# Performance work log

Hardware: AMD Instinct MI355X
Metric: run time of the kernel (lower is better)

Reference implementation:

```python
import jax, jax.numpy as jnp
import numpy as np

B, A, NBH, F, G, H = 8, 512, 64, 128, 50, 8
DH = F // H
CUTOFF = 5.0


def setup_inputs() -> dict:
    key = jax.random.key(0)
    ks = jax.random.split(key, 13)
    x = jax.random.normal(ks[0], (B, A, F), jnp.float32)
    e = jax.random.normal(ks[1], (B, A, F), jnp.float32)
    t = jax.random.normal(ks[2], (B, F), jnp.float32)
    # distances in [0, 1.2*cutoff] so some pairs fall outside the cutoff
    r_ij = jax.random.uniform(ks[3], (B, A, NBH), jnp.float32) * (1.2 * CUTOFF)
    f_ij = jax.random.normal(ks[4], (B, A, NBH, G), jnp.float32)
    neighbors = jax.random.randint(ks[5], (B, A, NBH), 0, A, jnp.int32)
    neighbor_mask = jax.random.randint(ks[6], (B, A, NBH), 0, 2, jnp.int32).astype(bool)
    sF = 1.0 / np.sqrt(F).astype(np.float32)
    W_filt = jax.random.normal(ks[7], (G, F), jnp.float32) * (1.0 / np.sqrt(G).astype(np.float32))
    b_filt = jnp.zeros((F,), jnp.float32)
    Wq = jax.random.normal(ks[8], (F, F), jnp.float32) * sF
    Wk = jax.random.normal(ks[9], (F, F), jnp.float32) * sF
    Wv = jax.random.normal(ks[10], (F, F), jnp.float32) * sF
    Wo = jax.random.normal(ks[11], (F, F), jnp.float32) * sF
    bo = jnp.zeros((F,), jnp.float32)
    return dict(e=e, x=x, t=t, r_ij=r_ij, f_ij=f_ij,
                W_filt=W_filt, b_filt=b_filt, Wq=Wq, Wk=Wk, Wv=Wv, Wo=Wo, bo=bo,
                neighbors=neighbors, neighbor_mask=neighbor_mask)


def reference(e, x, t, r_ij, f_ij, W_filt, b_filt, Wq, Wk, Wv, Wo, bo,
              neighbors, neighbor_mask):
    # ---- filter network + cosine cutoff: W (B, A, NBH, F) ----
    W = f_ij @ W_filt + b_filt
    C = 0.5 * (jnp.cos(jnp.pi * r_ij / CUTOFF) + 1.0)
    C = C * (r_ij < CUTOFF).astype(x.dtype)           # (B, A, NBH)
    W = W * C[..., None]

    # ---- neighbor gather: nbh (B, A, NBH, F) ----
    bidx = jnp.arange(B)[:, None, None]
    nbh = x[bidx, neighbors]                           # irregular gather
    nbh = nbh * W                                      # filter-modulated messages

    # ---- EgoAttention: central atom queries its neighbors ----
    q = (x @ Wq).reshape(B, A, H, DH)                  # bahd
    k = (nbh @ Wk).reshape(B, A, NBH, H, DH)           # banhd
    v = (nbh @ Wv).reshape(B, A, NBH, H, DH)
    scale = np.float32(1.0 / np.sqrt(DH))
    scores = jnp.einsum('bahd,banhd->bahn', q, k) * scale
    scores = jnp.where(neighbor_mask[:, :, None, :], scores, jnp.float32(-1e9))
    attn = jax.nn.softmax(scores, axis=-1)             # over neighbors
    msg = jnp.einsum('bahn,banhd->bahd', attn, v).reshape(B, A, F)
    v_out = msg @ Wo + bo

    # ---- residual (apply_transition_function=False branch) ----
    return x + v_out
```

## Files before the change

### kernel.cpp

```cpp
#include <hip/hip_runtime.h>
#include <math.h>

#define BB 8
#define AA 512
#define NBH 64
#define FF 128
#define GG 50
#define CUTOFF 5.0f

typedef __attribute__((ext_vector_type(8)))  short bf16x8;
typedef __attribute__((ext_vector_type(4)))  float f32x4;
typedef __attribute__((ext_vector_type(16))) float f32x16;

#define MST 136

#define WV_OFF   0
#define WO_OFF   16384
#define WQ_OFF   32768
#define WKT_OFF  49152
#define WF_OFF   65536
#define XB_OFF   73728
#define KQ_OFF   598016
#define PACK_ELEMS 598016
#define PACK_BLOCKS (PACK_ELEMS / 256)
#define QK_BLOCKS  1024

__device__ __forceinline__ short f2bf(float f) {
    union { float f; unsigned u; } v; v.f = f;
    unsigned r = v.u + 0x7fffu + ((v.u >> 16) & 1u);
    return (short)(r >> 16);
}
__device__ __forceinline__ short f2bf_fast(float f) {
    return (short)((__float_as_uint(f) + 0x8000u) >> 16);
}
__device__ __forceinline__ unsigned int pk2bf(float a, float b) {
    unsigned int ua = __float_as_uint(a) + 0x8000u;
    unsigned int ub = __float_as_uint(b) + 0x8000u;
    return __builtin_amdgcn_perm(ub, ua, 0x07060302u);
}
__device__ __forceinline__ bf16x8 ld_f8_bfpk(const float* p) {
    const float2* p2 = (const float2*)p;
    float2 a = p2[0], b = p2[1], c = p2[2], d = p2[3];
    union { unsigned int u[4]; bf16x8 v; } r;
    r.u[0] = pk2bf(a.x, a.y);
    r.u[1] = pk2bf(b.x, b.y);
    r.u[2] = pk2bf(c.x, c.y);
    r.u[3] = pk2bf(d.x, d.y);
    return r.v;
}
__device__ __forceinline__ int swz(int n) { return ((n >> 3) & 3) << 3; }

__global__ void pack_kernel(const float* __restrict__ Wk,
                            const float* __restrict__ Wv,
                            const float* __restrict__ Wq,
                            const float* __restrict__ Wo,
                            const float* __restrict__ Wf,
                            const float* __restrict__ b_filt,
                            const float* __restrict__ x,
                            short* __restrict__ ws)
{
    int gid = blockIdx.x * blockDim.x + threadIdx.x;
    if (gid < 16384) {
        int idx = gid;
        int j = idx & 7, l = (idx >> 3) & 63, rest = idx >> 9;
        int s = rest & 7, w = rest >> 3;
        int k = 16 * s + ((l >> 5) << 3) + j;
        int n = 32 * w + (l & 31);
        ws[WV_OFF + idx] = f2bf(Wv[k * FF + n]);
    } else if (gid < 65536) {
        int which = (gid - 16384) >> 14;
        int idx = (gid - 16384) & 16383;
        int j = idx & 7, l = (idx >> 3) & 63, rest = idx >> 9;
        int s = rest & 3, c = rest >> 2;
        int k = 32 * s + (l >> 4) * 8 + j;
        int n = 16 * c + (l & 15);
        float v;
        if (which == 0)      v = Wo[k * FF + n];
        else if (which == 1) v = Wq[k * FF + n];
        else                 v = Wk[n * FF + k];
        ws[WO_OFF + which * 16384 + idx] = f2bf(v);
    } else if (gid < 73728) {
        int idx = gid - 65536;
        int j = idx & 7, l = (idx >> 3) & 63, rest = idx >> 9;
        int s = rest & 3, w = rest >> 2;
        int k = 16 * s + ((l >> 5) << 3) + j;
        int n = 32 * w + (l & 31);
        float v = (k < GG) ? Wf[k * FF + n] : (k == GG ? b_filt[n] : 0.0f);
        ws[WF_OFF + idx] = f2bf(v);
    } else {
        int idx = gid - XB_OFF;
        ws[XB_OFF + idx] = f2bf(x[idx]);
    }
}

__global__ __launch_bounds__(256)
void qk_kernel(const short* __restrict__ xB,
               const short* __restrict__ WqB,
               const short* __restrict__ WktB,
               short* __restrict__ kqc)
{
    const int tid  = threadIdx.x;
    const int lane = tid & 63;
    const int w    = tid >> 6;
    const int a    = blockIdx.x * 4 + w;
    const int l15  = lane & 15;
    const int quad = lane >> 4;

    __shared__ short qls[4][128];

    {
        const short* xbrow = &xB[(size_t)a * FF];
        bf16x8 xa[4];
#pragma unroll
        for (int s = 0; s < 4; ++s)
            xa[s] = *(const bf16x8*)&xbrow[32 * s + quad * 8];
#pragma unroll
        for (int cg = 0; cg < 8; ++cg) {
            f32x4 z = {0.f, 0.f, 0.f, 0.f};
#pragma unroll
            for (int s = 0; s < 4; ++s) {
                bf16x8 bq = *(const bf16x8*)&WqB[((cg * 4 + s) * 64 + lane) * 8];
                z = __builtin_amdgcn_mfma_f32_16x16x32_bf16(xa[s], bq, z, 0, 0, 0);
            }
            if (quad == 0) qls[w][cg * 16 + l15] = f2bf_fast(z[0] * 0.25f);
        }
    }
    __syncthreads();

    {
        short* kqa = kqc + (size_t)a * 1024;
        bf16x8 zero8;
#pragma unroll
        for (int jj = 0; jj < 8; ++jj) zero8[jj] = 0;
        bf16x8 ap[4];
#pragma unroll
        for (int s = 0; s < 4; ++s) {
            bf16x8 qoct = *(const bf16x8*)&qls[w][32 * s + quad * 8];
            int h8 = 2 * s + (quad >> 1);
            ap[s] = (l15 == h8) ? qoct : zero8;
        }
#pragma unroll
        for (int ct = 0; ct < 8; ++ct) {
            f32x4 z = {0.f, 0.f, 0.f, 0.f};
#pragma unroll
            for (int s = 0; s < 4; ++s) {
                bf16x8 bk = *(const bf16x8*)&WktB[((ct * 4 + s) * 64 + lane) * 8];
                z = __builtin_amdgcn_mfma_f32_16x16x32_bf16(ap[s], bk, z, 0, 0, 0);
            }
            if (quad < 2) {
#pragma unroll
                for (int r = 0; r < 4; ++r) {
                    int h = quad * 4 + r;
                    kqa[h * 128 + ct * 16 + l15] = f2bf_fast(z[r]);
                }
            }
        }
    }
}

__global__ __launch_bounds__(256, 4)
void tdt_main(const float* __restrict__ x,
              const float* __restrict__ r_ij,
              const float* __restrict__ f_ij,
              const float* __restrict__ bo,
              const int*   __restrict__ neighbors,
              const int*   __restrict__ nmask,
              const short* __restrict__ WvB,
              const short* __restrict__ WoB,
              const short* __restrict__ WfB,
              const short* __restrict__ xB,
              const short* __restrict__ kqc,
              float* __restrict__ out)
{
    const int ba   = blockIdx.x;
    const int b    = ba >> 9;
    const int tid  = threadIdx.x;
    const int lane = tid & 63;
    const int w    = tid >> 6;
    const int l15  = lane & 15;
    const int quad = lane >> 4;
    const int l31  = lane & 31;
    const int khalf = (lane >> 5) << 3;
    const int w5_4  = (lane >> 5) * 4;

    __shared__ short M_s[NBH * MST];
    __shared__ short msg_bf[FF];

    const float* xrow = x + (size_t)ba * FF;
    const unsigned short* xbu = (const unsigned short*)xB + (size_t)b * AA * FF;
    const size_t bao = (size_t)ba;

    int   nbr_reg = neighbors[bao * NBH + lane];
    float C_reg;
    {
        float r = r_ij[bao * NBH + lane];
        float c = 0.5f * (__cosf((float)M_PI * r * (1.0f / CUTOFF)) + 1.0f);
        C_reg = (r < CUTOFF) ? c : 0.0f;
    }
    unsigned long long mask64 = __ballot(nmask[bao * NBH + lane] != 0);

    {
        const float* fm0 = f_ij + bao * (size_t)(NBH * GG) + (size_t)l31 * GG;
        int c = 32 * w + l31;
#pragma unroll
        for (int mt = 0; mt < 2; ++mt) {
            f32x16 wacc;
#pragma unroll
            for (int r = 0; r < 16; ++r) wacc[r] = 0.0f;
            const float* fm = fm0 + mt * 32 * GG;
#pragma unroll
            for (int s = 0; s < 4; ++s) {
                bf16x8 bfw = *(const bf16x8*)&WfB[((w * 4 + s) * 64 + lane) * 8];
                bf16x8 fa;
                if (s < 3) {
                    fa = ld_f8_bfpk(fm + 16 * s + khalf);
                } else {
#pragma unroll
                    for (int jj = 0; jj < 8; ++jj) fa[jj] = 0;
                    if (lane < 32) {
                        fa[0] = f2bf_fast(fm[48]);
                        fa[1] = f2bf_fast(fm[49]);
                        fa[2] = (short)0x3F80;
                    }
                }
                wacc = __builtin_amdgcn_mfma_f32_32x32x16_bf16(fa, bfw, wacc, 0, 0, 0);
            }
#pragma unroll
            for (int r = 0; r < 16; ++r) {
                int   n   = 32 * mt + (r & 3) + 8 * (r >> 2) + w5_4;
                int   nbn = __shfl(nbr_reg, n, 64);
                float cn  = __shfl(C_reg, n, 64);
                float xv  = __uint_as_float((unsigned)xbu[(size_t)nbn * FF + c] << 16);
                M_s[n * MST + (c ^ swz(n))] = f2bf_fast(wacc[r] * cn * xv);
            }
        }
    }
    __syncthreads();

    float sum = 0.0f, acc = 0.0f;
    const short* kqa = kqc + (size_t)ba * 1024 + (size_t)(2 * w + ((lane >> 4) & 1)) * 128;
#pragma unroll
    for (int mt = 0; mt < 2; ++mt) {
        int m = 32 * mt + l31;
        f32x16 sacc, vacc;
#pragma unroll
        for (int r = 0; r < 16; ++r) { sacc[r] = 0.0f; vacc[r] = 0.0f; }
#pragma unroll
        for (int s = 0; s < 8; ++s) {
            bf16x8 ma = *(const bf16x8*)&M_s[m * MST + ((16 * s + khalf) ^ swz(m))];
            bf16x8 bq = *(const bf16x8*)&kqa[16 * s + khalf];
            bf16x8 bv = *(const bf16x8*)&WvB[((w * 8 + s) * 64 + lane) * 8];
            sacc = __builtin_amdgcn_mfma_f32_32x32x16_bf16(ma, bq, sacc, 0, 0, 0);
            vacc = __builtin_amdgcn_mfma_f32_32x32x16_bf16(ma, bv, vacc, 0, 0, 0);
        }
#pragma unroll
        for (int r = 0; r < 16; ++r) {
            int   n = 32 * mt + (r & 3) + 8 * (r >> 2) + w5_4;
            float e = ((mask64 >> n) & 1ull) ? __expf(sacc[r]) : 0.0f;
            sum += e;
            acc  = fmaf(e, vacc[r], acc);
        }
    }
    sum += __shfl_xor(sum, 32, 64);
    acc += __shfl_xor(acc, 32, 64);
    if (lane < 32) msg_bf[32 * w + l31] = f2bf_fast(acc / sum);
    __syncthreads();

    {
        bf16x8 mga[4];
#pragma unroll
        for (int s = 0; s < 4; ++s)
            mga[s] = *(const bf16x8*)&msg_bf[s * 32 + quad * 8];
#pragma unroll
        for (int ct = 0; ct < 2; ++ct) {
            int cg = 2 * w + ct;
            f32x4 z = {0.f, 0.f, 0.f, 0.f};
#pragma unroll
            for (int s = 0; s < 4; ++s) {
                bf16x8 bw = *(const bf16x8*)&WoB[((cg * 4 + s) * 64 + lane) * 8];
                z = __builtin_amdgcn_mfma_f32_16x16x32_bf16(mga[s], bw, z, 0, 0, 0);
            }
            if (quad == 0) {
                int col = cg * 16 + l15;
                out[bao * FF + col] = z[0] + xrow[col] + bo[col];
            }
        }
    }
}

extern "C" void kernel_launch(void* const* d_in, const int* in_sizes, int n_in,
                              void* d_out, int out_size, void* d_ws, size_t ws_size,
                              hipStream_t stream) {
    const float* x      = (const float*)d_in[1];
    const float* r_ij   = (const float*)d_in[3];
    const float* f_ij   = (const float*)d_in[4];
    const float* W_filt = (const float*)d_in[5];
    const float* b_filt = (const float*)d_in[6];
    const float* Wq     = (const float*)d_in[7];
    const float* Wk     = (const float*)d_in[8];
    const float* Wv     = (const float*)d_in[9];
    const float* Wo     = (const float*)d_in[10];
    const float* bo     = (const float*)d_in[11];
    const int*   nbr    = (const int*)d_in[12];
    const int*   msk    = (const int*)d_in[13];
    float* out = (float*)d_out;

    short* ws   = (short*)d_ws;
    short* WvB  = ws + WV_OFF;
    short* WoB  = ws + WO_OFF;
    short* WqB  = ws + WQ_OFF;
    short* WktB = ws + WKT_OFF;
    short* WfB  = ws + WF_OFF;
    short* xB   = ws + XB_OFF;
    short* kqc  = ws + KQ_OFF;

    hipLaunchKernelGGL(pack_kernel, dim3(PACK_BLOCKS), dim3(256), 0, stream,
                       Wk, Wv, Wq, Wo, W_filt, b_filt, x, ws);
    hipLaunchKernelGGL(qk_kernel, dim3(QK_BLOCKS), dim3(256), 0, stream,
                       xB, WqB, WktB, kqc);
    hipLaunchKernelGGL(tdt_main, dim3(BB * AA), dim3(256), 0, stream,
                       x, r_ij, f_ij, bo, nbr, msk,
                       WvB, WoB, WfB, xB, kqc, out);
}
```

Before: 170.7 us.

## Merge weight packing and q/k projection into one prep kernel, drop bf16 x copy

```diff
diff --git a/kernel.cpp b/kernel.cpp
--- a/kernel.cpp
+++ b/kernel.cpp
@@ -16,12 +16,9 @@
 
 #define WV_OFF   0
 #define WO_OFF   16384
-#define WQ_OFF   32768
-#define WKT_OFF  49152
-#define WF_OFF   65536
-#define XB_OFF   73728
-#define KQ_OFF   598016
-#define PACK_ELEMS 598016
+#define WF_OFF   32768
+#define KQ_OFF   40960
+#define PACK_ELEMS 40960
 #define PACK_BLOCKS (PACK_ELEMS / 256)
 #define QK_BLOCKS  1024
 
@@ -50,7 +47,7 @@
 }
 __device__ __forceinline__ int swz(int n) { return ((n >> 3) & 3) << 3; }
 
-__global__ void pack_kernel(const float* __restrict__ Wk,
+__global__ void prep_kernel(const float* __restrict__ Wk,
                             const float* __restrict__ Wv,
                             const float* __restrict__ Wq,
                             const float* __restrict__ Wo,
@@ -59,67 +56,59 @@
                             const float* __restrict__ x,
                             short* __restrict__ ws)
 {
-    int gid = blockIdx.x * blockDim.x + threadIdx.x;
-    if (gid < 16384) {
-        int idx = gid;
-        int j = idx & 7, l = (idx >> 3) & 63, rest = idx >> 9;
-        int s = rest & 7, w = rest >> 3;
-        int k = 16 * s + ((l >> 5) << 3) + j;
-        int n = 32 * w + (l & 31);
-        ws[WV_OFF + idx] = f2bf(Wv[k * FF + n]);
-    } else if (gid < 65536) {
-        int which = (gid - 16384) >> 14;
-        int idx = (gid - 16384) & 16383;
-        int j = idx & 7, l = (idx >> 3) & 63, rest = idx >> 9;
-        int s = rest & 3, c = rest >> 2;
-        int k = 32 * s + (l >> 4) * 8 + j;
-        int n = 16 * c + (l & 15);
-        float v;
-        if (which == 0)      v = Wo[k * FF + n];
-        else if (which == 1) v = Wq[k * FF + n];
-        else                 v = Wk[n * FF + k];
-        ws[WO_OFF + which * 16384 + idx] = f2bf(v);
-    } else if (gid < 73728) {
-        int idx = gid - 65536;
-        int j = idx & 7, l = (idx >> 3) & 63, rest = idx >> 9;
-        int s = rest & 3, w = rest >> 2;
-        int k = 16 * s + ((l >> 5) << 3) + j;
-        int n = 32 * w + (l & 31);
-        float v = (k < GG) ? Wf[k * FF + n] : (k == GG ? b_filt[n] : 0.0f);
-        ws[WF_OFF + idx] = f2bf(v);
-    } else {
-        int idx = gid - XB_OFF;
-        ws[XB_OFF + idx] = f2bf(x[idx]);
-    }
-}
-
-__global__ __launch_bounds__(256)
-void qk_kernel(const short* __restrict__ xB,
-               const short* __restrict__ WqB,
-               const short* __restrict__ WktB,
-               short* __restrict__ kqc)
-{
-    const int tid  = threadIdx.x;
+    const int bid = blockIdx.x;
+    const int tid = threadIdx.x;
+
+    __shared__ short qls[4][128];
+
+    if (bid < PACK_BLOCKS) {
+        int gid = bid * 256 + tid;
+        if (gid < 16384) {
+            int idx = gid;
+            int j = idx & 7, l = (idx >> 3) & 63, rest = idx >> 9;
+            int s = rest & 7, w = rest >> 3;
+            int k = 16 * s + ((l >> 5) << 3) + j;
+            int n = 32 * w + (l & 31);
+            ws[WV_OFF + idx] = f2bf(Wv[k * FF + n]);
+        } else if (gid < 32768) {
+            int idx = gid - 16384;
+            int j = idx & 7, l = (idx >> 3) & 63, rest = idx >> 9;
+            int s = rest & 3, c = rest >> 2;
+            int k = 32 * s + (l >> 4) * 8 + j;
+            int n = 16 * c + (l & 15);
+            ws[WO_OFF + idx] = f2bf(Wo[k * FF + n]);
+        } else {
+            int idx = gid - 32768;
+            int j = idx & 7, l = (idx >> 3) & 63, rest = idx >> 9;
+            int s = rest & 3, w = rest >> 2;
+            int k = 16 * s + ((l >> 5) << 3) + j;
+            int n = 32 * w + (l & 31);
+            float v = (k < GG) ? Wf[k * FF + n] : (k == GG ? b_filt[n] : 0.0f);
+            ws[WF_OFF + idx] = f2bf(v);
+        }
+        return;
+    }
+
+    const int w    = tid >> 6;
     const int lane = tid & 63;
-    const int w    = tid >> 6;
-    const int a    = blockIdx.x * 4 + w;
+    const int a    = (bid - PACK_BLOCKS) * 4 + w;
     const int l15  = lane & 15;
     const int quad = lane >> 4;
 
-    __shared__ short qls[4][128];
-
-    {
-        const short* xbrow = &xB[(size_t)a * FF];
+    {
         bf16x8 xa[4];
 #pragma unroll
         for (int s = 0; s < 4; ++s)
-            xa[s] = *(const bf16x8*)&xbrow[32 * s + quad * 8];
+            xa[s] = ld_f8_bfpk(x + (size_t)a * FF + 32 * s + quad * 8);
 #pragma unroll
         for (int cg = 0; cg < 8; ++cg) {
             f32x4 z = {0.f, 0.f, 0.f, 0.f};
 #pragma unroll
             for (int s = 0; s < 4; ++s) {
-                bf16x8 bq = *(const bf16x8*)&WqB[((cg * 4 + s) * 64 + lane) * 8];
+                const float* wq = Wq + (size_t)(32 * s + quad * 8) * FF + 16 * cg + l15;
+                bf16x8 bq;
+#pragma unroll
+                for (int j = 0; j < 8; ++j) bq[j] = f2bf_fast(wq[j * FF]);
                 z = __builtin_amdgcn_mfma_f32_16x16x32_bf16(xa[s], bq, z, 0, 0, 0);
             }
             if (quad == 0) qls[w][cg * 16 + l15] = f2bf_fast(z[0] * 0.25f);
@@ -128,7 +117,7 @@
     __syncthreads();
 
     {
-        short* kqa = kqc + (size_t)a * 1024;
+        short* kqa = ws + KQ_OFF + (size_t)a * 1024;
         bf16x8 zero8;
 #pragma unroll
         for (int jj = 0; jj < 8; ++jj) zero8[jj] = 0;
@@ -144,7 +133,7 @@
             f32x4 z = {0.f, 0.f, 0.f, 0.f};
 #pragma unroll
             for (int s = 0; s < 4; ++s) {
-                bf16x8 bk = *(const bf16x8*)&WktB[((ct * 4 + s) * 64 + lane) * 8];
+                bf16x8 bk = ld_f8_bfpk(Wk + (size_t)(16 * ct + l15) * FF + 32 * s + quad * 8);
                 z = __builtin_amdgcn_mfma_f32_16x16x32_bf16(ap[s], bk, z, 0, 0, 0);
             }
             if (quad < 2) {
@@ -168,7 +157,6 @@
               const short* __restrict__ WvB,
               const short* __restrict__ WoB,
               const short* __restrict__ WfB,
-              const short* __restrict__ xB,
               const short* __restrict__ kqc,
               float* __restrict__ out)
 {
@@ -187,8 +175,8 @@
     __shared__ short msg_bf[FF];
 
     const float* xrow = x + (size_t)ba * FF;
-    const unsigned short* xbu = (const unsigned short*)xB + (size_t)b * AA * FF;
-    const size_t bao = (size_t)ba;
+    const float* xb   = x + (size_t)b * AA * FF;
+    const size_t bao  = (size_t)ba;
 
     int   nbr_reg = neighbors[bao * NBH + lane];
     float C_reg;
@@ -230,7 +218,7 @@
                 int   n   = 32 * mt + (r & 3) + 8 * (r >> 2) + w5_4;
                 int   nbn = __shfl(nbr_reg, n, 64);
                 float cn  = __shfl(C_reg, n, 64);
-                float xv  = __uint_as_float((unsigned)xbu[(size_t)nbn * FF + c] << 16);
+                float xv  = xb[(size_t)nbn * FF + c];
                 M_s[n * MST + (c ^ swz(n))] = f2bf_fast(wacc[r] * cn * xv);
             }
         }
@@ -305,20 +293,15 @@
     const int*   msk    = (const int*)d_in[13];
     float* out = (float*)d_out;
 
-    short* ws   = (short*)d_ws;
-    short* WvB  = ws + WV_OFF;
-    short* WoB  = ws + WO_OFF;
-    short* WqB  = ws + WQ_OFF;
-    short* WktB = ws + WKT_OFF;
-    short* WfB  = ws + WF_OFF;
-    short* xB   = ws + XB_OFF;
-    short* kqc  = ws + KQ_OFF;
-
-    hipLaunchKernelGGL(pack_kernel, dim3(PACK_BLOCKS), dim3(256), 0, stream,
+    short* ws  = (short*)d_ws;
+    short* WvB = ws + WV_OFF;
+    short* WoB = ws + WO_OFF;
+    short* WfB = ws + WF_OFF;
+    short* kqc = ws + KQ_OFF;
+
+    hipLaunchKernelGGL(prep_kernel, dim3(PACK_BLOCKS + QK_BLOCKS), dim3(256), 0, stream,
                        Wk, Wv, Wq, Wo, W_filt, b_filt, x, ws);
-    hipLaunchKernelGGL(qk_kernel, dim3(QK_BLOCKS), dim3(256), 0, stream,
-                       xB, WqB, WktB, kqc);
     hipLaunchKernelGGL(tdt_main, dim3(BB * AA), dim3(256), 0, stream,
                        x, r_ij, f_ij, bo, nbr, msk,
-                       WvB, WoB, WfB, xB, kqc, out);
-}
+                       WvB, WoB, WfB, kqc, out);
+}
```

Result: slower. 193.1 us (+13.1%).
